# Kernel tuning notes

Hardware: AMD Instinct MI355X
Metric: run time of the kernel (lower is better)

## Reference

```python
import jax, jax.numpy as jnp
import numpy as np

N = 100000      # num_node
D = 64          # latent_dim
R_EX = 8        # num_relation_ex
R_IM = 4        # num_relation_im
E_EX = 2000000  # explicit edges
E_IM = 1000000  # implicit edges


def setup_inputs() -> dict:
    key = jax.random.key(0)
    ks = jax.random.split(key, 32)
    f = lambda i, shape, s=0.05: jax.random.normal(ks[i], shape, dtype=jnp.float32) * s
    inp = {}
    inp["edge_index_ex"] = jax.random.randint(ks[0], (2, E_EX), 0, N)
    inp["edge_type_ex"] = jax.random.randint(ks[1], (E_EX,), 0, R_EX)
    inp["edge_index_im"] = jax.random.randint(ks[2], (2, E_IM), 0, N)
    inp["edge_type_im"] = jax.random.randint(ks[3], (E_IM,), 0, R_IM)
    # RGCN layer-1 (in_channels = num_node, x=None -> weight acts as per-relation embedding table)
    inp["W1_ex"] = f(4, (R_EX, N, D)); inp["root1_ex"] = f(5, (N, D)); inp["b1_ex"] = f(6, (D,))
    inp["W1_im"] = f(7, (R_IM, N, D)); inp["root1_im"] = f(8, (N, D)); inp["b1_im"] = f(9, (D,))
    # RGCN layer-2 (latent_dim -> latent_dim)
    inp["W2_ex"] = f(10, (R_EX, D, D)); inp["root2_ex"] = f(11, (D, D)); inp["b2_ex"] = f(12, (D,))
    inp["W2_im"] = f(13, (R_IM, D, D)); inp["root2_im"] = f(14, (D, D)); inp["b2_im"] = f(15, (D,))
    # ATTITU fusion head: four Linear(D, 1)
    inp["att_w11"] = f(16, (D,)); inp["att_b11"] = f(17, ())
    inp["att_w12"] = f(18, (D,)); inp["att_b12"] = f(19, ())
    inp["att_w21"] = f(20, (D,)); inp["att_b21"] = f(21, ())
    inp["att_w22"] = f(22, (D,)); inp["att_b22"] = f(23, ())
    # MLP aggregation: Linear(2D, D) -> LeakyReLU -> Linear(D, D)
    inp["agg_W1"] = f(24, (2 * D, D)); inp["agg_b1"] = f(25, (D,))
    inp["agg_W2"] = f(26, (D, D)); inp["agg_b2"] = f(27, (D,))
    return inp


def _rgcn_embed(W, root, bias, src, dst, etype, R):
    # Layer 1, x=None: out_i = root_i + bias + sum_r mean_{e: type(e)=r, dst(e)=i} W[r, src(e)]
    out = root + bias  # [N, D]
    for r in range(R):
        m = (etype == r).astype(jnp.float32)            # [E]
        msg = W[r][src] * m[:, None]                    # [E, D] relation-r embedding gather
        s = jax.ops.segment_sum(msg, dst, num_segments=N)
        c = jax.ops.segment_sum(m, dst, num_segments=N)
        out = out + s / jnp.maximum(c, 1.0)[:, None]
    return out


def _rgcn(x, W, root, bias, src, dst, etype, R):
    # Layer 2: out_i = x_i @ root + bias + sum_r (mean_{e: type=r, dst=i} x[src(e)]) @ W[r]
    out = x @ root + bias
    for r in range(R):
        m = (etype == r).astype(x.dtype)
        msg = x[src] * m[:, None]                        # [E, D]
        s = jax.ops.segment_sum(msg, dst, num_segments=N)
        c = jax.ops.segment_sum(m, dst, num_segments=N)
        h = s / jnp.maximum(c, 1.0)[:, None]             # mean-aggregated, then linear (PyG order)
        out = out + h @ W[r]
    return out


def _attitu(e1, e2, w11, b11, w12, b12, w21, b21, w22, b22):
    s1 = jax.nn.softmax(jnp.stack([e1 @ w11 + b11, e2 @ w12 + b12], axis=1), axis=1)  # [N, 2]
    f1 = s1[:, 0:1] * e1 + s1[:, 1:2] * e2
    s2 = jax.nn.softmax(jnp.stack([e1 @ w21 + b21, e2 @ w22 + b22], axis=1), axis=1)
    f2 = s2[:, 1:2] * e2 + s2[:, 0:1] * e1
    return f1, f2


def reference(edge_index_ex, edge_type_ex, edge_index_im, edge_type_im,
              W1_ex, root1_ex, b1_ex, W1_im, root1_im, b1_im,
              W2_ex, root2_ex, b2_ex, W2_im, root2_im, b2_im,
              att_w11, att_b11, att_w12, att_b12, att_w21, att_b21, att_w22, att_b22,
              agg_W1, agg_b1, agg_W2, agg_b2):
    src_ex, dst_ex = edge_index_ex[0], edge_index_ex[1]
    src_im, dst_im = edge_index_im[0], edge_index_im[1]
    ex_x1 = _rgcn_embed(W1_ex, root1_ex, b1_ex, src_ex, dst_ex, edge_type_ex, R_EX)
    im_x1 = _rgcn_embed(W1_im, root1_im, b1_im, src_im, dst_im, edge_type_im, R_IM)
    t_ex, t_im = _attitu(ex_x1, im_x1, att_w11, att_b11, att_w12, att_b12,
                         att_w21, att_b21, att_w22, att_b22)
    ex_x2 = _rgcn(t_ex, W2_ex, root2_ex, b2_ex, src_ex, dst_ex, edge_type_ex, R_EX)
    im_x2 = _rgcn(t_im, W2_im, root2_im, b2_im, src_im, dst_im, edge_type_im, R_IM)
    cat = jnp.concatenate([ex_x1 + ex_x2, im_x1 + im_x2], axis=1)  # [N, 2D]
    return jax.nn.leaky_relu(cat @ agg_W1 + agg_b1, negative_slope=0.01) @ agg_W2 + agg_b2
```

## Files before the change

kernel.cpp:

```cpp
#include <hip/hip_runtime.h>
#include <hip/hip_bf16.h>

#define N_NODE 100000
#define DIM 64
#define R_EX 8
#define R_IM 4
#define E_EX 2000000
#define E_IM 1000000
#define ND (N_NODE * DIM)

typedef __hip_bfloat16 bf16;

__device__ __forceinline__ float b2f(bf16 v) { return __bfloat162float(v); }

__device__ __forceinline__ float ldv(const void* p, long long i, int f32) {
    return f32 ? ((const float*)p)[i] : b2f(((const bf16*)p)[i]);
}

__global__ void detect_kernel(const void* probe, int* flag) {
    int t = threadIdx.x;
    float v = b2f(((const bf16*)probe)[t]);
    int bad = !(fabsf(v) <= 4.0f);
    unsigned long long m = __ballot(bad);
    if (t == 0) *flag = (m != 0ull) ? 1 : 0;
}

__global__ void count_kernel(const int* __restrict__ eidx, const int* __restrict__ etype,
                             float* __restrict__ cnt, int E) {
    int e = blockIdx.x * blockDim.x + threadIdx.x;
    if (e >= E) return;
    int dst = eidx[E + e];
    int r = etype[e];
    atomicAdd(&cnt[r * N_NODE + dst], 1.0f);
}

__global__ void inv_kernel(float* __restrict__ cnt, int n) {
    int i = blockIdx.x * blockDim.x + threadIdx.x;
    if (i >= n) return;
    cnt[i] = 1.0f / fmaxf(cnt[i], 1.0f);
}

__global__ void l1_init(const void* __restrict__ root, const void* __restrict__ bias,
                        const int* __restrict__ fp, float* __restrict__ x1) {
    int i = blockIdx.x * blockDim.x + threadIdx.x;
    if (i >= ND) return;
    int f32 = *fp;
    x1[i] = ldv(root, i, f32) + ldv(bias, i & (DIM - 1), f32);
}

__global__ void l1_edge(const int* __restrict__ eidx, const int* __restrict__ etype,
                        const void* __restrict__ W1, const float* __restrict__ inv,
                        const int* __restrict__ fp, float* __restrict__ x1, int E) {
    int gid = blockIdx.x * blockDim.x + threadIdx.x;
    int e = gid >> 6;
    int d = gid & 63;
    if (e >= E) return;
    int f32 = *fp;
    int src = eidx[e];
    int dst = eidx[E + e];
    int r = etype[e];
    float w = inv[r * N_NODE + dst];
    float v = ldv(W1, ((long long)r * N_NODE + src) * DIM + d, f32);
    atomicAdd(&x1[dst * DIM + d], v * w);
}

__global__ void attitu_kernel(const float* __restrict__ ex1, const float* __restrict__ im1,
                              const void* __restrict__ w11, const void* __restrict__ b11,
                              const void* __restrict__ w12, const void* __restrict__ b12,
                              const void* __restrict__ w21, const void* __restrict__ b21,
                              const void* __restrict__ w22, const void* __restrict__ b22,
                              const int* __restrict__ fp,
                              float* __restrict__ t_ex, float* __restrict__ t_im) {
    int gid = blockIdx.x * blockDim.x + threadIdx.x;
    int i = gid >> 6;
    int d = gid & 63;
    if (i >= N_NODE) return;
    int f32 = *fp;
    float e1 = ex1[i * DIM + d];
    float e2 = im1[i * DIM + d];
    float p11 = e1 * ldv(w11, d, f32);
    float p12 = e2 * ldv(w12, d, f32);
    float p21 = e1 * ldv(w21, d, f32);
    float p22 = e2 * ldv(w22, d, f32);
#pragma unroll
    for (int off = 32; off; off >>= 1) {
        p11 += __shfl_xor(p11, off);
        p12 += __shfl_xor(p12, off);
        p21 += __shfl_xor(p21, off);
        p22 += __shfl_xor(p22, off);
    }
    float a11 = p11 + ldv(b11, 0, f32);
    float a12 = p12 + ldv(b12, 0, f32);
    float a21 = p21 + ldv(b21, 0, f32);
    float a22 = p22 + ldv(b22, 0, f32);

    float m1 = fmaxf(a11, a12);
    float z11 = __expf(a11 - m1), z12 = __expf(a12 - m1);
    float i1 = 1.0f / (z11 + z12);
    float s10 = z11 * i1, s11 = z12 * i1;

    float m2 = fmaxf(a21, a22);
    float z21 = __expf(a21 - m2), z22 = __expf(a22 - m2);
    float i2 = 1.0f / (z21 + z22);
    float s20 = z21 * i2, s21 = z22 * i2;

    t_ex[i * DIM + d] = s10 * e1 + s11 * e2;
    t_im[i * DIM + d] = s20 * e1 + s21 * e2;
}

__global__ void l2_init_fused(const float* __restrict__ t, const void* __restrict__ root2,
                              const void* __restrict__ b2, const int* __restrict__ fp,
                              float* __restrict__ x1) {
    int gid = blockIdx.x * blockDim.x + threadIdx.x;
    int i = gid >> 6;
    int d = gid & 63;
    if (i >= N_NODE) return;
    int f32 = *fp;
    float tv = t[i * DIM + d];
    float acc = ldv(b2, d, f32) + x1[i * DIM + d];
    if (f32) {
        const float* W = (const float*)root2;
#pragma unroll
        for (int k = 0; k < DIM; ++k) acc += __shfl(tv, k) * W[k * DIM + d];
    } else {
        const bf16* W = (const bf16*)root2;
#pragma unroll
        for (int k = 0; k < DIM; ++k) acc += __shfl(tv, k) * b2f(W[k * DIM + d]);
    }
    x1[i * DIM + d] = acc;
}

__global__ void l2_edge(const int* __restrict__ eidx, const int* __restrict__ etype,
                        const float* __restrict__ t, const void* __restrict__ W2,
                        const float* __restrict__ inv, const int* __restrict__ fp,
                        float* __restrict__ a2, int E) {
    int gid = blockIdx.x * blockDim.x + threadIdx.x;
    int e = gid >> 6;
    int d = gid & 63;
    if (e >= E) return;
    int f32 = *fp;
    int src = eidx[e];
    int dst = eidx[E + e];
    int r = etype[e];
    float tv = t[src * DIM + d];
    float acc = 0.0f;
    if (f32) {
        const float* W = (const float*)W2 + r * DIM * DIM;
#pragma unroll
        for (int k = 0; k < DIM; ++k) acc += __shfl(tv, k) * W[k * DIM + d];
    } else {
        const bf16* W = (const bf16*)W2 + r * DIM * DIM;
#pragma unroll
        for (int k = 0; k < DIM; ++k) acc += __shfl(tv, k) * b2f(W[k * DIM + d]);
    }
    float w = inv[r * N_NODE + dst];
    atomicAdd(&a2[dst * DIM + d], acc * w);
}

__global__ void final_kernel(const float* __restrict__ a2ex, const float* __restrict__ a2im,
                             const void* __restrict__ aggW1, const void* __restrict__ aggb1,
                             const void* __restrict__ aggW2, const void* __restrict__ aggb2,
                             const int* __restrict__ fp, void* __restrict__ out) {
    int gid = blockIdx.x * blockDim.x + threadIdx.x;
    int i = gid >> 6;
    int d = gid & 63;
    if (i >= N_NODE) return;
    int f32 = *fp;
    float cex = a2ex[i * DIM + d];
    float cim = a2im[i * DIM + d];
    float h = ldv(aggb1, d, f32);
    if (f32) {
        const float* W = (const float*)aggW1;
#pragma unroll
        for (int k = 0; k < DIM; ++k) {
            h += __shfl(cex, k) * W[k * DIM + d];
            h += __shfl(cim, k) * W[(DIM + k) * DIM + d];
        }
    } else {
        const bf16* W = (const bf16*)aggW1;
#pragma unroll
        for (int k = 0; k < DIM; ++k) {
            h += __shfl(cex, k) * b2f(W[k * DIM + d]);
            h += __shfl(cim, k) * b2f(W[(DIM + k) * DIM + d]);
        }
    }
    h = (h > 0.0f) ? h : 0.01f * h;
    float o = ldv(aggb2, d, f32);
    if (f32) {
        const float* W = (const float*)aggW2;
#pragma unroll
        for (int k = 0; k < DIM; ++k) o += __shfl(h, k) * W[k * DIM + d];
        ((float*)out)[i * DIM + d] = o;
    } else {
        const bf16* W = (const bf16*)aggW2;
#pragma unroll
        for (int k = 0; k < DIM; ++k) o += __shfl(h, k) * b2f(W[k * DIM + d]);
        ((bf16*)out)[i * DIM + d] = __float2bfloat16(o);
    }
}

extern "C" void kernel_launch(void* const* d_in, const int* in_sizes, int n_in,
                              void* d_out, int out_size, void* d_ws, size_t ws_size,
                              hipStream_t stream) {
    const int* eidx_ex  = (const int*)d_in[0];
    const int* etype_ex = (const int*)d_in[1];
    const int* eidx_im  = (const int*)d_in[2];
    const int* etype_im = (const int*)d_in[3];
    const void* W1_ex   = d_in[4];
    const void* root1_ex= d_in[5];
    const void* b1_ex   = d_in[6];
    const void* W1_im   = d_in[7];
    const void* root1_im= d_in[8];
    const void* b1_im   = d_in[9];
    const void* W2_ex   = d_in[10];
    const void* root2_ex= d_in[11];
    const void* b2_ex   = d_in[12];
    const void* W2_im   = d_in[13];
    const void* root2_im= d_in[14];
    const void* b2_im   = d_in[15];
    const void* att_w11 = d_in[16];
    const void* att_b11 = d_in[17];
    const void* att_w12 = d_in[18];
    const void* att_b12 = d_in[19];
    const void* att_w21 = d_in[20];
    const void* att_b21 = d_in[21];
    const void* att_w22 = d_in[22];
    const void* att_b22 = d_in[23];
    const void* agg_W1  = d_in[24];
    const void* agg_b1  = d_in[25];
    const void* agg_W2  = d_in[26];
    const void* agg_b2  = d_in[27];

    float* ws = (float*)d_ws;
    int*   flag   = (int*)d_ws;
    float* inv_ex = ws + 64;
    float* inv_im = inv_ex + R_EX * N_NODE;
    float* x1ex   = inv_im + R_IM * N_NODE;
    float* x1im   = x1ex + ND;
    float* t_ex   = x1im + ND;
    float* t_im   = t_ex + ND;

    const int B = 256;

    detect_kernel<<<1, 64, 0, stream>>>(b1_ex, flag);

    hipMemsetAsync(inv_ex, 0, (size_t)(R_EX + R_IM) * N_NODE * sizeof(float), stream);
    count_kernel<<<(E_EX + B - 1) / B, B, 0, stream>>>(eidx_ex, etype_ex, inv_ex, E_EX);
    count_kernel<<<(E_IM + B - 1) / B, B, 0, stream>>>(eidx_im, etype_im, inv_im, E_IM);
    inv_kernel<<<((R_EX + R_IM) * N_NODE + B - 1) / B, B, 0, stream>>>(inv_ex, (R_EX + R_IM) * N_NODE);

    l1_init<<<(ND + B - 1) / B, B, 0, stream>>>(root1_ex, b1_ex, flag, x1ex);
    l1_init<<<(ND + B - 1) / B, B, 0, stream>>>(root1_im, b1_im, flag, x1im);
    l1_edge<<<(E_EX * 64) / B, B, 0, stream>>>(eidx_ex, etype_ex, W1_ex, inv_ex, flag, x1ex, E_EX);
    l1_edge<<<(E_IM * 64) / B, B, 0, stream>>>(eidx_im, etype_im, W1_im, inv_im, flag, x1im, E_IM);

    attitu_kernel<<<(N_NODE * 64 + B - 1) / B, B, 0, stream>>>(
        x1ex, x1im, att_w11, att_b11, att_w12, att_b12, att_w21, att_b21, att_w22, att_b22,
        flag, t_ex, t_im);

    l2_init_fused<<<(N_NODE * 64 + B - 1) / B, B, 0, stream>>>(t_ex, root2_ex, b2_ex, flag, x1ex);
    l2_init_fused<<<(N_NODE * 64 + B - 1) / B, B, 0, stream>>>(t_im, root2_im, b2_im, flag, x1im);
    l2_edge<<<(E_EX * 64) / B, B, 0, stream>>>(eidx_ex, etype_ex, t_ex, W2_ex, inv_ex, flag, x1ex, E_EX);
    l2_edge<<<(E_IM * 64) / B, B, 0, stream>>>(eidx_im, etype_im, t_im, W2_im, inv_im, flag, x1im, E_IM);

    final_kernel<<<(N_NODE * 64 + B - 1) / B, B, 0, stream>>>(
        x1ex, x1im, agg_W1, agg_b1, agg_W2, agg_b2, flag, (void*)d_out);
}
```

Measured before the change: 3.662 ms.

## Aggregate layer-2 messages per relation before applying relation weights

Layer 2 used to multiply each edge's source feature by its relation matrix and then scatter the result. It now first scatter-adds raw source features into per-relation node buffers, then applies each relation's 64x64 weight and the inverse degree once per node. This swaps per-edge matmul work (E times 64x64) for per-node matmul work (N times R). The price is extra workspace, memsets and passes over the edges when workspace limits how many relations fit at once.

```diff
diff --git a/kernel.cpp b/kernel.cpp
--- a/kernel.cpp
+++ b/kernel.cpp
@@ -128,6 +128,47 @@
         for (int k = 0; k < DIM; ++k) acc += __shfl(tv, k) * b2f(W[k * DIM + d]);
     }
     x1[i * DIM + d] = acc;
+}
+
+__global__ void l2_agg(const int* __restrict__ eidx, const int* __restrict__ etype,
+                       const float* __restrict__ t, float* __restrict__ h,
+                       int E, int r0, int rc) {
+    int gid = blockIdx.x * blockDim.x + threadIdx.x;
+    int e = gid >> 6;
+    int d = gid & 63;
+    if (e >= E) return;
+    int r = etype[e] - r0;
+    if ((unsigned)r >= (unsigned)rc) return;
+    int src = eidx[e];
+    int dst = eidx[E + e];
+    atomicAdd(&h[(long long)r * ND + dst * DIM + d], t[src * DIM + d]);
+}
+
+__global__ void l2_dense(const float* __restrict__ h, const void* __restrict__ W2,
+                         const float* __restrict__ inv, const int* __restrict__ fp,
+                         float* __restrict__ a2, int r0, int rc) {
+    int gid = blockIdx.x * blockDim.x + threadIdx.x;
+    int i = gid >> 6;
+    int d = gid & 63;
+    if (i >= N_NODE) return;
+    int f32 = *fp;
+    float acc = a2[i * DIM + d];
+    for (int c = 0; c < rc; ++c) {
+        float hv = h[(long long)c * ND + i * DIM + d];
+        float w = inv[(r0 + c) * N_NODE + i];
+        float s = 0.0f;
+        if (f32) {
+            const float* W = (const float*)W2 + (r0 + c) * DIM * DIM;
+#pragma unroll
+            for (int k = 0; k < DIM; ++k) s += __shfl(hv, k) * W[k * DIM + d];
+        } else {
+            const bf16* W = (const bf16*)W2 + (r0 + c) * DIM * DIM;
+#pragma unroll
+            for (int k = 0; k < DIM; ++k) s += __shfl(hv, k) * b2f(W[k * DIM + d]);
+        }
+        acc += w * s;
+    }
+    a2[i * DIM + d] = acc;
 }
 
 __global__ void l2_edge(const int* __restrict__ eidx, const int* __restrict__ etype,
@@ -239,6 +280,12 @@
     float* x1im   = x1ex + ND;
     float* t_ex   = x1im + ND;
     float* t_im   = t_ex + ND;
+    float* hbuf   = t_im + ND;
+
+    const long long base_floats = 64 + (long long)(R_EX + R_IM) * N_NODE + 4LL * ND;
+    long long avail = (long long)(ws_size / sizeof(float)) - base_floats;
+    int cmax = (avail > 0) ? (int)(avail / ND) : 0;
+    if (cmax > R_EX) cmax = R_EX;
 
     const int B = 256;
 
@@ -260,8 +307,24 @@
 
     l2_init_fused<<<(N_NODE * 64 + B - 1) / B, B, 0, stream>>>(t_ex, root2_ex, b2_ex, flag, x1ex);
     l2_init_fused<<<(N_NODE * 64 + B - 1) / B, B, 0, stream>>>(t_im, root2_im, b2_im, flag, x1im);
-    l2_edge<<<(E_EX * 64) / B, B, 0, stream>>>(eidx_ex, etype_ex, t_ex, W2_ex, inv_ex, flag, x1ex, E_EX);
-    l2_edge<<<(E_IM * 64) / B, B, 0, stream>>>(eidx_im, etype_im, t_im, W2_im, inv_im, flag, x1im, E_IM);
+
+    if (cmax >= 1) {
+        for (int r0 = 0; r0 < R_EX; r0 += cmax) {
+            int rc = (R_EX - r0 < cmax) ? (R_EX - r0) : cmax;
+            hipMemsetAsync(hbuf, 0, (size_t)rc * ND * sizeof(float), stream);
+            l2_agg<<<(E_EX * 64) / B, B, 0, stream>>>(eidx_ex, etype_ex, t_ex, hbuf, E_EX, r0, rc);
+            l2_dense<<<(N_NODE * 64 + B - 1) / B, B, 0, stream>>>(hbuf, W2_ex, inv_ex, flag, x1ex, r0, rc);
+        }
+        for (int r0 = 0; r0 < R_IM; r0 += cmax) {
+            int rc = (R_IM - r0 < cmax) ? (R_IM - r0) : cmax;
+            hipMemsetAsync(hbuf, 0, (size_t)rc * ND * sizeof(float), stream);
+            l2_agg<<<(E_IM * 64) / B, B, 0, stream>>>(eidx_im, etype_im, t_im, hbuf, E_IM, r0, rc);
+            l2_dense<<<(N_NODE * 64 + B - 1) / B, B, 0, stream>>>(hbuf, W2_im, inv_im, flag, x1im, r0, rc);
+        }
+    } else {
+        l2_edge<<<(E_EX * 64) / B, B, 0, stream>>>(eidx_ex, etype_ex, t_ex, W2_ex, inv_ex, flag, x1ex, E_EX);
+        l2_edge<<<(E_IM * 64) / B, B, 0, stream>>>(eidx_im, etype_im, t_im, W2_im, inv_im, flag, x1im, E_IM);
+    }
 
     final_kernel<<<(N_NODE * 64 + B - 1) / B, B, 0, stream>>>(
         x1ex, x1im, agg_W1, agg_b1, agg_W2, agg_b2, flag, (void*)d_out);
```

New measurement: 3.233 ms. 1.13x faster.
